# Optimization experiments

Measured on AMD Instinct MI355X. Metric: run time of the kernel, lower is better.

Reference implementation:

```python
import jax, jax.numpy as jnp
import numpy as np

DIM = 256          # args.dim
MAX_Z = 100        # args.max_z
N_ATOM_EMBED = DIM - 1  # Euclidean manifold: dim - 1
B, N = 256, 128    # graphs, nodes per graph
E = B * N * N      # fully connected edges per batch, flattened
NORM_CONSTANT = 1.0


def setup_inputs() -> dict:
    key = jax.random.key(0)
    ks = jax.random.split(key, 8)
    x = jax.random.normal(ks[0], (B, N, 3), dtype=jnp.float32)
    categories = jax.random.randint(ks[1], (B, N), 0, MAX_Z)
    charges = jax.random.normal(ks[2], (B, N, 1), dtype=jnp.float32)
    edges = jax.random.randint(ks[3], (2, E), 0, B * N)
    node_mask = jnp.ones((B, N, 1), dtype=jnp.float32)
    edge_mask = jnp.ones((E, 1), dtype=jnp.float32)
    # nn.Embedding(max_z, n_atom_embed, padding_idx=0): row 0 is zeros
    emb = jax.random.normal(ks[4], (MAX_Z, N_ATOM_EMBED), dtype=jnp.float32)
    emb_table = emb.at[0].set(0.0)
    # nn.Linear(dim, 2*dim)
    lim = 1.0 / np.sqrt(DIM)
    W = jax.random.uniform(ks[5], (DIM, 2 * DIM), minval=-lim, maxval=lim, dtype=jnp.float32)
    b_lin = jax.random.uniform(ks[6], (2 * DIM,), minval=-lim, maxval=lim, dtype=jnp.float32)
    return {"x": x, "categories": categories, "charges": charges, "edges": edges,
            "node_mask": node_mask, "edge_mask": edge_mask,
            "emb_table": emb_table, "W": W, "b_lin": b_lin}


def coord2diff(x, edges, norm_constant=NORM_CONSTANT):
    row, col = edges[0], edges[1]
    coord_diff = x[row] - x[col]                              # [E, 3] gather + diff
    radial = jnp.sum(coord_diff * coord_diff, axis=1, keepdims=True)  # [E, 1]
    norm = jnp.sqrt(radial + 1e-8)
    coord_diff = coord_diff / (norm + norm_constant)
    return radial, coord_diff


def reference(x, categories, charges, edges, node_mask, edge_mask, emb_table, W, b_lin):
    h = emb_table[categories]                      # [B, N, dim-1] embedding lookup
    h = jnp.concatenate([charges, h], axis=2)      # [B, N, dim]
    b, n_nodes, d = h.shape
    xf = x.reshape(b * n_nodes, 3)
    nm = node_mask.reshape(b * n_nodes, 1)
    h = h.reshape(b * n_nodes, d) * nm             # masked node features
    radial, coord_diff = coord2diff(xf, edges)     # edge-index gather + norm
    # encode() pass-through (abstract layers treated as identity), then head
    parameters = h @ W + b_lin                     # [B*N, 2*dim] mean/logvar
    return parameters, radial, coord_diff
```

## Files before the change

### kernel.cpp

```cpp
#include <hip/hip_runtime.h>

typedef unsigned short u16;
typedef unsigned int u32;
typedef __attribute__((ext_vector_type(8))) short bf16x8;
typedef __attribute__((ext_vector_type(4))) float f32x4;

#define DIM 256
#define NOUT 512
#define MROWS 32768
#define NEDGE (256*128*128)
#define PARAM_SZ (32768*512)

__device__ __forceinline__ u16 f2bf(float f) {
    u32 x = __float_as_uint(f);
    u32 r = (x + 0x7FFFu + ((x >> 16) & 1u)) >> 16;
    return (u16)r;
}

__global__ __launch_bounds__(1024) void transpose_kernel(const float* __restrict__ W,
                                                         u16* __restrict__ Wt) {
    __shared__ u16 tile[32][33];
    int n0 = blockIdx.x * 32;
    int k0 = blockIdx.y * 32;
    int tx = threadIdx.x, ty = threadIdx.y;
    tile[ty][tx] = f2bf(W[(k0 + ty) * NOUT + n0 + tx]);
    __syncthreads();
    Wt[(n0 + ty) * DIM + k0 + tx] = tile[tx][ty];
}

__global__ __launch_bounds__(256) void edge_kernel(const int* __restrict__ edges,
                                                   const float* __restrict__ x,
                                                   float* __restrict__ radial_out,
                                                   float* __restrict__ cd_out) {
    int e = blockIdx.x * 256 + threadIdx.x;
    int row = edges[e];
    int col = edges[NEDGE + e];
    float ax = x[row * 3 + 0], ay = x[row * 3 + 1], az = x[row * 3 + 2];
    float bx = x[col * 3 + 0], by = x[col * 3 + 1], bz = x[col * 3 + 2];
    float dx = ax - bx, dy = ay - by, dz = az - bz;
    float radial = dx * dx + dy * dy + dz * dz;
    float denom = sqrtf(radial + 1e-8f) + 1.0f;
    radial_out[e] = radial;

    __shared__ float buf[768];
    buf[threadIdx.x * 3 + 0] = dx / denom;
    buf[threadIdx.x * 3 + 1] = dy / denom;
    buf[threadIdx.x * 3 + 2] = dz / denom;
    __syncthreads();
    size_t base = (size_t)blockIdx.x * 768;
    cd_out[base + threadIdx.x]       = buf[threadIdx.x];
    cd_out[base + 256 + threadIdx.x] = buf[256 + threadIdx.x];
    cd_out[base + 512 + threadIdx.x] = buf[512 + threadIdx.x];
}

__global__ __launch_bounds__(256, 2) void gemm_kernel(const int* __restrict__ cats,
                                                      const float* __restrict__ charges,
                                                      const float* __restrict__ nmask,
                                                      const float* __restrict__ emb,
                                                      const u16* __restrict__ Wt,
                                                      const float* __restrict__ bias,
                                                      float* __restrict__ out) {
    __shared__ u16 h_lds[64][DIM + 8];
    const int m0 = blockIdx.x * 64;
    const int tid = threadIdx.x;

    for (int t = tid; t < 1024; t += 256) {
        int r = t >> 4;
        int c0 = (t & 15) * 16;
        int m = m0 + r;
        float mask = nmask[m];
        int ebase = cats[m] * (DIM - 1);
        #pragma unroll
        for (int i = 0; i < 16; ++i) {
            int c = c0 + i;
            float v = (c == 0) ? charges[m] : emb[ebase + c - 1];
            h_lds[r][c] = f2bf(v * mask);
        }
    }
    __syncthreads();

    const int wave = tid >> 6;
    const int lane = tid & 63;
    const int lrow = lane & 15;
    const int quad = lane >> 4;
    const int nbase = wave * 128;

    f32x4 acc[4][8];
    #pragma unroll
    for (int ms = 0; ms < 4; ++ms)
        #pragma unroll
        for (int nt = 0; nt < 8; ++nt) acc[ms][nt] = (f32x4)(0.0f);

    #pragma unroll
    for (int k0 = 0; k0 < DIM; k0 += 32) {
        bf16x8 a[4];
        #pragma unroll
        for (int ms = 0; ms < 4; ++ms)
            a[ms] = *(const bf16x8*)&h_lds[ms * 16 + lrow][k0 + quad * 8];
        #pragma unroll
        for (int nt = 0; nt < 8; ++nt) {
            bf16x8 bfr = *(const bf16x8*)&Wt[(size_t)(nbase + nt * 16 + lrow) * DIM + k0 + quad * 8];
            #pragma unroll
            for (int ms = 0; ms < 4; ++ms)
                acc[ms][nt] = __builtin_amdgcn_mfma_f32_16x16x32_bf16(a[ms], bfr, acc[ms][nt], 0, 0, 0);
        }
    }

    #pragma unroll
    for (int nt = 0; nt < 8; ++nt) {
        int n = nbase + nt * 16 + lrow;
        float bv = bias[n];
        #pragma unroll
        for (int ms = 0; ms < 4; ++ms)
            #pragma unroll
            for (int r = 0; r < 4; ++r)
                out[(size_t)(m0 + ms * 16 + quad * 4 + r) * NOUT + n] = acc[ms][nt][r] + bv;
    }
}

extern "C" void kernel_launch(void* const* d_in, const int* in_sizes, int n_in,
                              void* d_out, int out_size, void* d_ws, size_t ws_size,
                              hipStream_t stream) {
    const float* x       = (const float*)d_in[0];
    const int*   cats    = (const int*)d_in[1];
    const float* charges = (const float*)d_in[2];
    const int*   edges   = (const int*)d_in[3];
    const float* nmask   = (const float*)d_in[4];
    const float* emb     = (const float*)d_in[6];
    const float* W       = (const float*)d_in[7];
    const float* bias    = (const float*)d_in[8];

    float* out    = (float*)d_out;
    float* params = out;
    float* radial = out + PARAM_SZ;
    float* cd     = out + PARAM_SZ + NEDGE;
    u16*   Wt     = (u16*)d_ws;

    transpose_kernel<<<dim3(16, 8), dim3(32, 32), 0, stream>>>(W, Wt);
    edge_kernel<<<NEDGE / 256, 256, 0, stream>>>(edges, x, radial, cd);
    gemm_kernel<<<MROWS / 64, 256, 0, stream>>>(cats, charges, nmask, emb, Wt, bias, params);
}
```

Baseline: 233.1 us.

## Pack coords to float4, pre-convert embedding to bf16, vectorize edge kernel

Adds a pack kernel that pads node coordinates to float4 and converts the embedding table to bf16 rows of 256 with a zero leading column. The edge kernel now handles four edges per thread using int4 index loads, single float4 gathers and float4 stores. The GEMM prologue copies whole pre-converted bf16 rows with 16-byte loads and only does the mask multiply when the mask is not one. This cuts scalar gather and store traffic and repeated conversion work, at the cost of an extra launch and extra workspace.

```diff
diff --git a/kernel.cpp b/kernel.cpp
--- a/kernel.cpp
+++ b/kernel.cpp
@@ -8,6 +8,7 @@
 #define DIM 256
 #define NOUT 512
 #define MROWS 32768
+#define NNODE 32768
 #define NEDGE (256*128*128)
 #define PARAM_SZ (32768*512)
 
@@ -15,6 +16,9 @@
     u32 x = __float_as_uint(f);
     u32 r = (x + 0x7FFFu + ((x >> 16) & 1u)) >> 16;
     return (u16)r;
+}
+__device__ __forceinline__ float bf2f(u16 u) {
+    union { u32 i; float f; } v; v.i = ((u32)u) << 16; return v.f;
 }
 
 __global__ __launch_bounds__(1024) void transpose_kernel(const float* __restrict__ W,
@@ -28,35 +32,66 @@
     Wt[(n0 + ty) * DIM + k0 + tx] = tile[tx][ty];
 }
 
+__global__ __launch_bounds__(256) void pack_kernel(const float* __restrict__ x,
+                                                   const float* __restrict__ emb,
+                                                   float4* __restrict__ xp,
+                                                   u16* __restrict__ embp) {
+    int i = blockIdx.x * 256 + threadIdx.x;
+    if (i < NNODE) {
+        float4 v;
+        v.x = x[i * 3 + 0]; v.y = x[i * 3 + 1]; v.z = x[i * 3 + 2]; v.w = 0.0f;
+        xp[i] = v;
+    }
+    if (i < 100 * 256) {
+        int col = i & 255;
+        int row = i >> 8;
+        embp[i] = (col == 0) ? (u16)0 : f2bf(emb[row * 255 + col - 1]);
+    }
+}
+
 __global__ __launch_bounds__(256) void edge_kernel(const int* __restrict__ edges,
-                                                   const float* __restrict__ x,
+                                                   const float4* __restrict__ xp,
                                                    float* __restrict__ radial_out,
                                                    float* __restrict__ cd_out) {
-    int e = blockIdx.x * 256 + threadIdx.x;
-    int row = edges[e];
-    int col = edges[NEDGE + e];
-    float ax = x[row * 3 + 0], ay = x[row * 3 + 1], az = x[row * 3 + 2];
-    float bx = x[col * 3 + 0], by = x[col * 3 + 1], bz = x[col * 3 + 2];
-    float dx = ax - bx, dy = ay - by, dz = az - bz;
-    float radial = dx * dx + dy * dy + dz * dz;
-    float denom = sqrtf(radial + 1e-8f) + 1.0f;
-    radial_out[e] = radial;
+    __shared__ float buf[3072];
+    const int tid = threadIdx.x;
+    const int t4 = blockIdx.x * 256 + tid;
+    int4 r4 = ((const int4*)edges)[t4];
+    int4 c4 = ((const int4*)(edges + NEDGE))[t4];
 
-    __shared__ float buf[768];
-    buf[threadIdx.x * 3 + 0] = dx / denom;
-    buf[threadIdx.x * 3 + 1] = dy / denom;
-    buf[threadIdx.x * 3 + 2] = dz / denom;
+    float4 xr0 = xp[r4.x], xr1 = xp[r4.y], xr2 = xp[r4.z], xr3 = xp[r4.w];
+    float4 xc0 = xp[c4.x], xc1 = xp[c4.y], xc2 = xp[c4.z], xc3 = xp[c4.w];
+
+    float4 rad;
+    float cdv[12];
+    #pragma unroll
+    for (int e = 0; e < 4; ++e) {
+        float4 a = (e == 0) ? xr0 : (e == 1) ? xr1 : (e == 2) ? xr2 : xr3;
+        float4 b = (e == 0) ? xc0 : (e == 1) ? xc1 : (e == 2) ? xc2 : xc3;
+        float dx = a.x - b.x, dy = a.y - b.y, dz = a.z - b.z;
+        float r = dx * dx + dy * dy + dz * dz;
+        float inv = 1.0f / (sqrtf(r + 1e-8f) + 1.0f);
+        ((float*)&rad)[e] = r;
+        cdv[e * 3 + 0] = dx * inv;
+        cdv[e * 3 + 1] = dy * inv;
+        cdv[e * 3 + 2] = dz * inv;
+    }
+    ((float4*)radial_out)[t4] = rad;
+
+    #pragma unroll
+    for (int k = 0; k < 3; ++k)
+        ((float4*)buf)[tid * 3 + k] = ((const float4*)cdv)[k];
     __syncthreads();
-    size_t base = (size_t)blockIdx.x * 768;
-    cd_out[base + threadIdx.x]       = buf[threadIdx.x];
-    cd_out[base + 256 + threadIdx.x] = buf[256 + threadIdx.x];
-    cd_out[base + 512 + threadIdx.x] = buf[512 + threadIdx.x];
+    float4* cdg = (float4*)(cd_out + (size_t)blockIdx.x * 3072);
+    #pragma unroll
+    for (int k = 0; k < 3; ++k)
+        cdg[k * 256 + tid] = ((const float4*)buf)[k * 256 + tid];
 }
 
 __global__ __launch_bounds__(256, 2) void gemm_kernel(const int* __restrict__ cats,
                                                       const float* __restrict__ charges,
                                                       const float* __restrict__ nmask,
-                                                      const float* __restrict__ emb,
+                                                      const u16* __restrict__ embp,
                                                       const u16* __restrict__ Wt,
                                                       const float* __restrict__ bias,
                                                       float* __restrict__ out) {
@@ -64,18 +99,34 @@
     const int m0 = blockIdx.x * 64;
     const int tid = threadIdx.x;
 
-    for (int t = tid; t < 1024; t += 256) {
-        int r = t >> 4;
-        int c0 = (t & 15) * 16;
+    {
+        int r = tid >> 2;
+        int q = tid & 3;
         int m = m0 + r;
         float mask = nmask[m];
-        int ebase = cats[m] * (DIM - 1);
+        const uint4* src = (const uint4*)(embp + (size_t)cats[m] * 256 + q * 64);
+        uint4 v[8];
         #pragma unroll
-        for (int i = 0; i < 16; ++i) {
-            int c = c0 + i;
-            float v = (c == 0) ? charges[m] : emb[ebase + c - 1];
-            h_lds[r][c] = f2bf(v * mask);
+        for (int t = 0; t < 8; ++t) v[t] = src[t];
+        if (mask != 1.0f) {
+            #pragma unroll
+            for (int t = 0; t < 8; ++t) {
+                u32* w = (u32*)&v[t];
+                #pragma unroll
+                for (int j = 0; j < 4; ++j) {
+                    u16 lo = f2bf(bf2f((u16)(w[j] & 0xFFFF)) * mask);
+                    u16 hi = f2bf(bf2f((u16)(w[j] >> 16)) * mask);
+                    w[j] = (u32)lo | ((u32)hi << 16);
+                }
+            }
         }
+        if (q == 0) {
+            u32* w0 = (u32*)&v[0];
+            w0[0] = (w0[0] & 0xFFFF0000u) | (u32)f2bf(charges[m] * mask);
+        }
+        #pragma unroll
+        for (int t = 0; t < 8; ++t)
+            *(uint4*)&h_lds[r][q * 64 + t * 8] = v[t];
     }
     __syncthreads();
 
@@ -134,9 +185,13 @@
     float* params = out;
     float* radial = out + PARAM_SZ;
     float* cd     = out + PARAM_SZ + NEDGE;
-    u16*   Wt     = (u16*)d_ws;
+
+    u16*    Wt   = (u16*)d_ws;
+    float4* xp   = (float4*)((char*)d_ws + 256 * 1024);
+    u16*    embp = (u16*)((char*)d_ws + 768 * 1024);
 
     transpose_kernel<<<dim3(16, 8), dim3(32, 32), 0, stream>>>(W, Wt);
-    edge_kernel<<<NEDGE / 256, 256, 0, stream>>>(edges, x, radial, cd);
-    gemm_kernel<<<MROWS / 64, 256, 0, stream>>>(cats, charges, nmask, emb, Wt, bias, params);
+    pack_kernel<<<NNODE / 256, 256, 0, stream>>>(x, emb, xp, embp);
+    edge_kernel<<<NEDGE / 1024, 256, 0, stream>>>(edges, xp, radial, cd);
+    gemm_kernel<<<MROWS / 64, 256, 0, stream>>>(cats, charges, nmask, embp, Wt, bias, params);
 }
```

After: 242.3 us. +4.0%, slower.
